# Optimization experiments

Measured on AMD Instinct MI355X. Metric: run time of the kernel, lower is better.

## Reference

```python
import jax, jax.numpy as jnp
import numpy as np

D_MODEL = 2048
RANK = 64
BATCH = 16384


def setup_inputs() -> dict:
    key = jax.random.key(0)
    ks = jax.random.split(key, 10)
    s = 1.0 / np.sqrt(D_MODEL)
    x = jax.random.normal(ks[0], (BATCH, D_MODEL), dtype=jnp.float32)
    state_re = jax.random.normal(ks[1], (BATCH, RANK), dtype=jnp.float32)
    state_im = jax.random.normal(ks[2], (BATCH, RANK), dtype=jnp.float32)
    W_dt = jax.random.uniform(ks[3], (RANK, D_MODEL), jnp.float32, -s, s)
    b_dt = jax.random.uniform(ks[4], (RANK,), jnp.float32, -s, s)
    W_ph = jax.random.uniform(ks[5], (RANK, D_MODEL), jnp.float32, -s, s)
    b_ph = jax.random.uniform(ks[6], (RANK,), jnp.float32, -s, s)
    W_B = jax.random.uniform(ks[7], (RANK, D_MODEL), jnp.float32, -s, s)
    sC = 1.0 / np.sqrt(RANK)
    W_C = jax.random.uniform(ks[8], (D_MODEL, RANK), jnp.float32, -sC, sC)
    A_real = jnp.log(jnp.arange(1, RANK + 1, dtype=jnp.float32))
    A_imag = jax.random.normal(ks[9], (RANK,), dtype=jnp.float32)
    return {"x": x, "state_re": state_re, "state_im": state_im,
            "W_dt": W_dt, "b_dt": b_dt, "W_ph": W_ph, "b_ph": b_ph,
            "W_B": W_B, "W_C": W_C, "A_real": A_real, "A_imag": A_imag}


def reference(x, state_re, state_im, W_dt, b_dt, W_ph, b_ph, W_B, W_C, A_real, A_imag):
    # four small GEMMs: [B, d_model] x [d_model, rank]
    dt = jax.nn.softplus(x @ W_dt.T + b_dt)                 # [B, rank]
    phase = jnp.tanh(x @ W_ph.T + b_ph) * jnp.pi            # [B, rank]
    decay = jnp.exp(-dt * jnp.exp(A_real))                  # [B, rank]
    angle = dt * A_imag + phase                              # [B, rank]
    B_val = x @ W_B.T                                        # [B, rank]
    cos = jnp.cos(angle)
    sin = jnp.sin(angle)
    # complex rotate-and-decay state update
    new_re = (state_re * cos - state_im * sin) * decay + B_val
    new_im = (state_re * sin + state_im * cos) * decay
    out = new_re @ W_C.T                                     # [B, d_model]
    return out, new_re, new_im
```

## Files before the change

### kernel.cpp

```cpp
#include <hip/hip_runtime.h>
#include <stdint.h>

#define D_MODEL 2048
#define RANK    64
#define BATCH   16384

#define BM      32
#define KSTEP   64
#define LDA     72

typedef unsigned short u16;
typedef __attribute__((ext_vector_type(8))) short  bf16x8;
typedef __attribute__((ext_vector_type(4))) float  f32x4;
typedef __attribute__((ext_vector_type(4))) unsigned short u16x4;
typedef __attribute__((ext_vector_type(8))) unsigned short u16x8;

#define P1_HI 0
#define P1_LO 393216
#define P2_HI 786432
#define P2_LO 917504

__device__ __forceinline__ u16 f2bf(float f) {
    uint32_t u = __float_as_uint(f);
    u += 0x7fffu + ((u >> 16) & 1u);
    return (u16)(u >> 16);
}
__device__ __forceinline__ float bf2f(u16 h) {
    return __uint_as_float(((uint32_t)h) << 16);
}

#define MFMA(a, b, c) __builtin_amdgcn_mfma_f32_16x16x32_bf16((a), (b), (c), 0, 0, 0)

__global__ __launch_bounds__(256) void prep_pack(
    const float* __restrict__ Wdt, const float* __restrict__ Wph,
    const float* __restrict__ WB,  const float* __restrict__ WC,
    u16* __restrict__ ws)
{
    const int t = blockIdx.x * 256 + threadIdx.x;
    const float* src;
    u16 *dhi, *dlo;
    if (t < 49152) {
        const int lane = t & 63;
        const int row  = (t >> 12) * 16 + (lane & 15);
        const int k0   = ((t >> 6) & 63) * 32 + (lane >> 4) * 8;
        src = (row < 64)  ? Wdt + row * 2048 + k0
            : (row < 128) ? Wph + (row - 64) * 2048 + k0
                          : WB  + (row - 128) * 2048 + k0;
        dhi = ws + P1_HI + t * 8;
        dlo = ws + P1_LO + t * 8;
    } else {
        const int t2   = t - 49152;
        const int lane = t2 & 63;
        const int row  = (t2 >> 7) * 16 + (lane & 15);
        const int k0   = ((t2 >> 6) & 1) * 32 + (lane >> 4) * 8;
        src = WC + row * 64 + k0;
        dhi = ws + P2_HI + t2 * 8;
        dlo = ws + P2_LO + t2 * 8;
    }
    const f32x4 a = *(const f32x4*)src;
    const f32x4 b = *(const f32x4*)(src + 4);
    u16x8 hi, lo;
    #pragma unroll
    for (int j = 0; j < 4; ++j) {
        hi[j]     = f2bf(a[j]);
        lo[j]     = f2bf(a[j] - bf2f(hi[j]));
        hi[4 + j] = f2bf(b[j]);
        lo[4 + j] = f2bf(b[j] - bf2f(hi[4 + j]));
    }
    *(u16x8*)dhi = hi;
    *(u16x8*)dlo = lo;
}

__global__ __launch_bounds__(256, 2) void mamba_fused(
    const float* __restrict__ x,
    const float* __restrict__ state_re, const float* __restrict__ state_im,
    const float* __restrict__ b_dt, const float* __restrict__ b_ph,
    const float* __restrict__ A_real, const float* __restrict__ A_imag,
    const u16* __restrict__ ws,
    float* __restrict__ dout)
{
    __shared__ __align__(16) u16 xa_hi[BM * LDA];
    __shared__ __align__(16) u16 xa_lo[BM * LDA];
    __shared__ __align__(16) u16 nr_hi[BM * LDA];
    __shared__ __align__(16) u16 nr_lo[BM * LDA];

    const u16* p1_hi = ws + P1_HI;
    const u16* p1_lo = ws + P1_LO;
    const u16* p2_hi = ws + P2_HI;
    const u16* p2_lo = ws + P2_LO;

    const int tid  = threadIdx.x;
    const int wg   = tid >> 6;
    const int lane = tid & 63;
    const int l15  = tid & 15;
    const int lg   = (tid & 63) >> 4;
    const int r0   = blockIdx.x * BM;

    const int srow = tid >> 3;
    const int skb  = (tid & 7) << 3;
    const float* xsrc = x + (size_t)(r0 + srow) * D_MODEL + skb;

    const int rb = wg * 16 + lg * 4;
    const int brow0 = r0 + l15;
    const int brow1 = r0 + 16 + l15;
    const f32x4 sre0 = *(const f32x4*)(state_re + (size_t)brow0 * RANK + rb);
    const f32x4 sre1 = *(const f32x4*)(state_re + (size_t)brow1 * RANK + rb);
    const f32x4 sim0 = *(const f32x4*)(state_im + (size_t)brow0 * RANK + rb);
    const f32x4 sim1 = *(const f32x4*)(state_im + (size_t)brow1 * RANK + rb);
    const f32x4 bdt4 = *(const f32x4*)(b_dt   + rb);
    const f32x4 bph4 = *(const f32x4*)(b_ph   + rb);
    const f32x4 Are4 = *(const f32x4*)(A_real + rb);
    const f32x4 Aim4 = *(const f32x4*)(A_imag + rb);

    f32x4 acc[3][2];
    #pragma unroll
    for (int g = 0; g < 3; ++g)
        #pragma unroll
        for (int m = 0; m < 2; ++m)
            acc[g][m] = (f32x4){0.f, 0.f, 0.f, 0.f};

    f32x4 va = *(const f32x4*)xsrc;
    f32x4 vb = *(const f32x4*)(xsrc + 4);

    for (int it = 0; it < D_MODEL / KSTEP; ++it) {
        f32x4 na = va, nb = vb;
        if (it < D_MODEL / KSTEP - 1) {
            na = *(const f32x4*)(xsrc + (it + 1) * KSTEP);
            nb = *(const f32x4*)(xsrc + (it + 1) * KSTEP + 4);
        }
        __syncthreads();
        {
            u16x4 h0, l0, h1, l1;
            #pragma unroll
            for (int j = 0; j < 4; ++j) {
                h0[j] = f2bf(va[j]);  l0[j] = f2bf(va[j] - bf2f(h0[j]));
                h1[j] = f2bf(vb[j]);  l1[j] = f2bf(vb[j] - bf2f(h1[j]));
            }
            *(u16x4*)(xa_hi + srow * LDA + skb)     = h0;
            *(u16x4*)(xa_hi + srow * LDA + skb + 4) = h1;
            *(u16x4*)(xa_lo + srow * LDA + skb)     = l0;
            *(u16x4*)(xa_lo + srow * LDA + skb + 4) = l1;
        }
        __syncthreads();
        #pragma unroll
        for (int kk = 0; kk < 2; ++kk) {
            const int klocal = kk * 32 + lg * 8;
            const bf16x8 xh0 = *(const bf16x8*)(xa_hi + l15 * LDA + klocal);
            const bf16x8 xl0 = *(const bf16x8*)(xa_lo + l15 * LDA + klocal);
            const bf16x8 xh1 = *(const bf16x8*)(xa_hi + (16 + l15) * LDA + klocal);
            const bf16x8 xl1 = *(const bf16x8*)(xa_lo + (16 + l15) * LDA + klocal);
            const int kwin = it * 2 + kk;
            #pragma unroll
            for (int g = 0; g < 3; ++g) {
                const int ntile = (g << 2) + wg;
                const size_t poff = (((size_t)ntile * 64 + kwin) * 64 + lane) * 8;
                const bf16x8 wh = *(const bf16x8*)(p1_hi + poff);
                const bf16x8 wl = *(const bf16x8*)(p1_lo + poff);
                acc[g][0] = MFMA(wh, xh0, acc[g][0]);
                acc[g][0] = MFMA(wl, xh0, acc[g][0]);
                acc[g][0] = MFMA(wh, xl0, acc[g][0]);
                acc[g][1] = MFMA(wh, xh1, acc[g][1]);
                acc[g][1] = MFMA(wl, xh1, acc[g][1]);
                acc[g][1] = MFMA(wh, xl1, acc[g][1]);
            }
        }
        va = na; vb = nb;
    }

    float* out_main = dout;
    float* out_nre  = dout + (size_t)BATCH * D_MODEL;
    float* out_nim  = out_nre + (size_t)BATCH * RANK;

    #pragma unroll
    for (int m = 0; m < 2; ++m) {
        const int   brow = m ? brow1 : brow0;
        const f32x4 sre4 = m ? sre1 : sre0;
        const f32x4 sim4 = m ? sim1 : sim0;
        f32x4 nre4, nim4;
        u16x4 nh4, nl4;
        #pragma unroll
        for (int j = 0; j < 4; ++j) {
            const float ydt = acc[0][m][j] + bdt4[j];
            const float dtv = fmaxf(ydt, 0.f) + log1pf(expf(-fabsf(ydt)));
            const float ph  = tanhf(acc[1][m][j] + bph4[j]) * 3.14159274101257324f;
            const float decay = expf(-dtv * expf(Are4[j]));
            const float angle = fmaf(dtv, Aim4[j], ph);
            float sn, cs;
            sincosf(angle, &sn, &cs);
            nre4[j] = (sre4[j] * cs - sim4[j] * sn) * decay + acc[2][m][j];
            nim4[j] = (sre4[j] * sn + sim4[j] * cs) * decay;
            const u16 h = f2bf(nre4[j]);
            nh4[j] = h;
            nl4[j] = f2bf(nre4[j] - bf2f(h));
        }
        *(f32x4*)(out_nre + (size_t)brow * RANK + rb) = nre4;
        *(f32x4*)(out_nim + (size_t)brow * RANK + rb) = nim4;
        *(u16x4*)(nr_hi + (m * 16 + l15) * LDA + rb) = nh4;
        *(u16x4*)(nr_lo + (m * 16 + l15) * LDA + rb) = nl4;
    }
    __syncthreads();

    bf16x8 nh[2][2], nl[2][2];
    #pragma unroll
    for (int m = 0; m < 2; ++m)
        #pragma unroll
        for (int kk = 0; kk < 2; ++kk) {
            const int off = (m * 16 + l15) * LDA + kk * 32 + lg * 8;
            nh[m][kk] = *(const bf16x8*)(nr_hi + off);
            nl[m][kk] = *(const bf16x8*)(nr_lo + off);
        }

    #pragma unroll 2
    for (int nt = 0; nt < 32; ++nt) {
        const int dtile = (wg << 5) + nt;
        bf16x8 ch[2], cl[2];
        #pragma unroll
        for (int kk = 0; kk < 2; ++kk) {
            const size_t poff = (((size_t)dtile * 2 + kk) * 64 + lane) * 8;
            ch[kk] = *(const bf16x8*)(p2_hi + poff);
            cl[kk] = *(const bf16x8*)(p2_lo + poff);
        }
        #pragma unroll
        for (int m = 0; m < 2; ++m) {
            f32x4 o = (f32x4){0.f, 0.f, 0.f, 0.f};
            #pragma unroll
            for (int kk = 0; kk < 2; ++kk) {
                o = MFMA(ch[kk], nh[m][kk], o);
                o = MFMA(cl[kk], nh[m][kk], o);
                o = MFMA(ch[kk], nl[m][kk], o);
            }
            const int brow = m ? brow1 : brow0;
            *(f32x4*)(out_main + (size_t)brow * D_MODEL + dtile * 16 + lg * 4) = o;
        }
    }
}

extern "C" void kernel_launch(void* const* d_in, const int* in_sizes, int n_in,
                              void* d_out, int out_size, void* d_ws, size_t ws_size,
                              hipStream_t stream)
{
    const float* x        = (const float*)d_in[0];
    const float* state_re = (const float*)d_in[1];
    const float* state_im = (const float*)d_in[2];
    const float* W_dt     = (const float*)d_in[3];
    const float* b_dt     = (const float*)d_in[4];
    const float* W_ph     = (const float*)d_in[5];
    const float* b_ph     = (const float*)d_in[6];
    const float* W_B      = (const float*)d_in[7];
    const float* W_C      = (const float*)d_in[8];
    const float* A_real   = (const float*)d_in[9];
    const float* A_imag   = (const float*)d_in[10];
    u16*   ws  = (u16*)d_ws;
    float* out = (float*)d_out;

    prep_pack<<<256, 256, 0, stream>>>(W_dt, W_ph, W_B, W_C, ws);
    mamba_fused<<<BATCH / BM, 256, 0, stream>>>(x, state_re, state_im, b_dt, b_ph,
                                                A_real, A_imag, ws, out);
}
```

Measured before the change: 361.5 us.

## Use 512-thread blocks with row-split warps and 256-wide K chunks

Each block now runs 8 waves: two row halves times four rank groups, so each wave owns one 16-row M tile instead of two. x is staged in 256-column chunks, which cuts the number of barrier pairs per block. The W_C fragments for the output GEMM are software-prefetched one tile ahead. The risk is that every weight fragment is now loaded by twice as many waves, doubling L2 traffic for the packed weights, and the larger LDS staging may limit occupancy.

```diff
diff --git a/kernel.cpp b/kernel.cpp
--- a/kernel.cpp
+++ b/kernel.cpp
@@ -6,8 +6,9 @@
 #define BATCH   16384
 
 #define BM      32
-#define KSTEP   64
-#define LDA     72
+#define CHUNK   256
+#define LDAC    264
+#define LDAN    72
 
 typedef unsigned short u16;
 typedef __attribute__((ext_vector_type(8))) short  bf16x8;
@@ -71,7 +72,7 @@
     *(u16x8*)dlo = lo;
 }
 
-__global__ __launch_bounds__(256, 2) void mamba_fused(
+__global__ __launch_bounds__(512, 4) void mamba_v3(
     const float* __restrict__ x,
     const float* __restrict__ state_re, const float* __restrict__ state_im,
     const float* __restrict__ b_dt, const float* __restrict__ b_ph,
@@ -79,10 +80,10 @@
     const u16* __restrict__ ws,
     float* __restrict__ dout)
 {
-    __shared__ __align__(16) u16 xa_hi[BM * LDA];
-    __shared__ __align__(16) u16 xa_lo[BM * LDA];
-    __shared__ __align__(16) u16 nr_hi[BM * LDA];
-    __shared__ __align__(16) u16 nr_lo[BM * LDA];
+    __shared__ __align__(16) u16 xa_hi[BM * LDAC];
+    __shared__ __align__(16) u16 xa_lo[BM * LDAC];
+    __shared__ __align__(16) u16 nr_hi[BM * LDAN];
+    __shared__ __align__(16) u16 nr_lo[BM * LDAN];
 
     const u16* p1_hi = ws + P1_HI;
     const u16* p1_lo = ws + P1_LO;
@@ -90,148 +91,151 @@
     const u16* p2_lo = ws + P2_LO;
 
     const int tid  = threadIdx.x;
-    const int wg   = tid >> 6;
+    const int w    = tid >> 6;
+    const int wm   = w >> 2;
+    const int wg   = w & 3;
     const int lane = tid & 63;
     const int l15  = tid & 15;
-    const int lg   = (tid & 63) >> 4;
+    const int lg   = lane >> 4;
     const int r0   = blockIdx.x * BM;
 
-    const int srow = tid >> 3;
-    const int skb  = (tid & 7) << 3;
-    const float* xsrc = x + (size_t)(r0 + srow) * D_MODEL + skb;
-
-    const int rb = wg * 16 + lg * 4;
-    const int brow0 = r0 + l15;
-    const int brow1 = r0 + 16 + l15;
-    const f32x4 sre0 = *(const f32x4*)(state_re + (size_t)brow0 * RANK + rb);
-    const f32x4 sre1 = *(const f32x4*)(state_re + (size_t)brow1 * RANK + rb);
-    const f32x4 sim0 = *(const f32x4*)(state_im + (size_t)brow0 * RANK + rb);
-    const f32x4 sim1 = *(const f32x4*)(state_im + (size_t)brow1 * RANK + rb);
+    const int srow = tid >> 4;
+    const int skc  = (tid & 15) << 4;
+    const float* xsrc = x + (size_t)(r0 + srow) * D_MODEL + skc;
+
+    const int brow_l = wm * 16 + l15;
+    const int brow   = r0 + brow_l;
+    const int rb     = wg * 16 + lg * 4;
+
+    f32x4 acc[3];
+    #pragma unroll
+    for (int g = 0; g < 3; ++g) acc[g] = (f32x4){0.f, 0.f, 0.f, 0.f};
+
+    f32x4 vx0 = *(const f32x4*)(xsrc);
+    f32x4 vx1 = *(const f32x4*)(xsrc + 4);
+    f32x4 vx2 = *(const f32x4*)(xsrc + 8);
+    f32x4 vx3 = *(const f32x4*)(xsrc + 12);
+
+    for (int c = 0; c < D_MODEL / CHUNK; ++c) {
+        __syncthreads();
+        {
+            u16x4 h, l;
+            #pragma unroll
+            for (int j = 0; j < 4; ++j) { h[j]=f2bf(vx0[j]); l[j]=f2bf(vx0[j]-bf2f(h[j])); }
+            *(u16x4*)(xa_hi + srow * LDAC + skc)      = h;
+            *(u16x4*)(xa_lo + srow * LDAC + skc)      = l;
+            #pragma unroll
+            for (int j = 0; j < 4; ++j) { h[j]=f2bf(vx1[j]); l[j]=f2bf(vx1[j]-bf2f(h[j])); }
+            *(u16x4*)(xa_hi + srow * LDAC + skc + 4)  = h;
+            *(u16x4*)(xa_lo + srow * LDAC + skc + 4)  = l;
+            #pragma unroll
+            for (int j = 0; j < 4; ++j) { h[j]=f2bf(vx2[j]); l[j]=f2bf(vx2[j]-bf2f(h[j])); }
+            *(u16x4*)(xa_hi + srow * LDAC + skc + 8)  = h;
+            *(u16x4*)(xa_lo + srow * LDAC + skc + 8)  = l;
+            #pragma unroll
+            for (int j = 0; j < 4; ++j) { h[j]=f2bf(vx3[j]); l[j]=f2bf(vx3[j]-bf2f(h[j])); }
+            *(u16x4*)(xa_hi + srow * LDAC + skc + 12) = h;
+            *(u16x4*)(xa_lo + srow * LDAC + skc + 12) = l;
+        }
+        __syncthreads();
+        if (c < D_MODEL / CHUNK - 1) {
+            const float* nsrc = xsrc + (c + 1) * CHUNK;
+            vx0 = *(const f32x4*)(nsrc);
+            vx1 = *(const f32x4*)(nsrc + 4);
+            vx2 = *(const f32x4*)(nsrc + 8);
+            vx3 = *(const f32x4*)(nsrc + 12);
+        }
+        #pragma unroll 2
+        for (int kw = 0; kw < CHUNK / 32; ++kw) {
+            const int xoff = brow_l * LDAC + kw * 32 + lg * 8;
+            const bf16x8 xh = *(const bf16x8*)(xa_hi + xoff);
+            const bf16x8 xl = *(const bf16x8*)(xa_lo + xoff);
+            const int kwin = c * (CHUNK / 32) + kw;
+            #pragma unroll
+            for (int g = 0; g < 3; ++g) {
+                const size_t poff = (((size_t)((g << 2) + wg) * 64 + kwin) * 64 + lane) * 8;
+                const bf16x8 wh = *(const bf16x8*)(p1_hi + poff);
+                const bf16x8 wl = *(const bf16x8*)(p1_lo + poff);
+                acc[g] = MFMA(wh, xh, acc[g]);
+                acc[g] = MFMA(wl, xh, acc[g]);
+                acc[g] = MFMA(wh, xl, acc[g]);
+            }
+        }
+    }
+
+    float* out_main = dout;
+    float* out_nre  = dout + (size_t)BATCH * D_MODEL;
+    float* out_nim  = out_nre + (size_t)BATCH * RANK;
+
+    const f32x4 sre4 = *(const f32x4*)(state_re + (size_t)brow * RANK + rb);
+    const f32x4 sim4 = *(const f32x4*)(state_im + (size_t)brow * RANK + rb);
     const f32x4 bdt4 = *(const f32x4*)(b_dt   + rb);
     const f32x4 bph4 = *(const f32x4*)(b_ph   + rb);
     const f32x4 Are4 = *(const f32x4*)(A_real + rb);
     const f32x4 Aim4 = *(const f32x4*)(A_imag + rb);
 
-    f32x4 acc[3][2];
-    #pragma unroll
-    for (int g = 0; g < 3; ++g)
-        #pragma unroll
-        for (int m = 0; m < 2; ++m)
-            acc[g][m] = (f32x4){0.f, 0.f, 0.f, 0.f};
-
-    f32x4 va = *(const f32x4*)xsrc;
-    f32x4 vb = *(const f32x4*)(xsrc + 4);
-
-    for (int it = 0; it < D_MODEL / KSTEP; ++it) {
-        f32x4 na = va, nb = vb;
-        if (it < D_MODEL / KSTEP - 1) {
-            na = *(const f32x4*)(xsrc + (it + 1) * KSTEP);
-            nb = *(const f32x4*)(xsrc + (it + 1) * KSTEP + 4);
-        }
-        __syncthreads();
-        {
-            u16x4 h0, l0, h1, l1;
-            #pragma unroll
-            for (int j = 0; j < 4; ++j) {
-                h0[j] = f2bf(va[j]);  l0[j] = f2bf(va[j] - bf2f(h0[j]));
-                h1[j] = f2bf(vb[j]);  l1[j] = f2bf(vb[j] - bf2f(h1[j]));
-            }
-            *(u16x4*)(xa_hi + srow * LDA + skb)     = h0;
-            *(u16x4*)(xa_hi + srow * LDA + skb + 4) = h1;
-            *(u16x4*)(xa_lo + srow * LDA + skb)     = l0;
-            *(u16x4*)(xa_lo + srow * LDA + skb + 4) = l1;
-        }
-        __syncthreads();
+    f32x4 nre4, nim4;
+    u16x4 nh4, nl4;
+    #pragma unroll
+    for (int j = 0; j < 4; ++j) {
+        const float ydt = acc[0][j] + bdt4[j];
+        const float dtv = fmaxf(ydt, 0.f) + log1pf(expf(-fabsf(ydt)));
+        const float ph  = tanhf(acc[1][j] + bph4[j]) * 3.14159274101257324f;
+        const float decay = expf(-dtv * expf(Are4[j]));
+        const float angle = fmaf(dtv, Aim4[j], ph);
+        float sn, cs;
+        sincosf(angle, &sn, &cs);
+        nre4[j] = (sre4[j] * cs - sim4[j] * sn) * decay + acc[2][j];
+        nim4[j] = (sre4[j] * sn + sim4[j] * cs) * decay;
+        const u16 h = f2bf(nre4[j]);
+        nh4[j] = h;
+        nl4[j] = f2bf(nre4[j] - bf2f(h));
+    }
+    *(f32x4*)(out_nre + (size_t)brow * RANK + rb) = nre4;
+    *(f32x4*)(out_nim + (size_t)brow * RANK + rb) = nim4;
+    *(u16x4*)(nr_hi + brow_l * LDAN + rb) = nh4;
+    *(u16x4*)(nr_lo + brow_l * LDAN + rb) = nl4;
+    __syncthreads();
+
+    bf16x8 nh[2], nl[2];
+    #pragma unroll
+    for (int kk = 0; kk < 2; ++kk) {
+        const int off = brow_l * LDAN + kk * 32 + lg * 8;
+        nh[kk] = *(const bf16x8*)(nr_hi + off);
+        nl[kk] = *(const bf16x8*)(nr_lo + off);
+    }
+
+    bf16x8 ch[2], cl[2], chn[2], cln[2];
+    {
+        const int dtile0 = wg << 5;
         #pragma unroll
         for (int kk = 0; kk < 2; ++kk) {
-            const int klocal = kk * 32 + lg * 8;
-            const bf16x8 xh0 = *(const bf16x8*)(xa_hi + l15 * LDA + klocal);
-            const bf16x8 xl0 = *(const bf16x8*)(xa_lo + l15 * LDA + klocal);
-            const bf16x8 xh1 = *(const bf16x8*)(xa_hi + (16 + l15) * LDA + klocal);
-            const bf16x8 xl1 = *(const bf16x8*)(xa_lo + (16 + l15) * LDA + klocal);
-            const int kwin = it * 2 + kk;
-            #pragma unroll
-            for (int g = 0; g < 3; ++g) {
-                const int ntile = (g << 2) + wg;
-                const size_t poff = (((size_t)ntile * 64 + kwin) * 64 + lane) * 8;
-                const bf16x8 wh = *(const bf16x8*)(p1_hi + poff);
-                const bf16x8 wl = *(const bf16x8*)(p1_lo + poff);
-                acc[g][0] = MFMA(wh, xh0, acc[g][0]);
-                acc[g][0] = MFMA(wl, xh0, acc[g][0]);
-                acc[g][0] = MFMA(wh, xl0, acc[g][0]);
-                acc[g][1] = MFMA(wh, xh1, acc[g][1]);
-                acc[g][1] = MFMA(wl, xh1, acc[g][1]);
-                acc[g][1] = MFMA(wh, xl1, acc[g][1]);
+            const size_t poff = (((size_t)dtile0 * 2 + kk) * 64 + lane) * 8;
+            ch[kk] = *(const bf16x8*)(p2_hi + poff);
+            cl[kk] = *(const bf16x8*)(p2_lo + poff);
+        }
+    }
+    for (int nt = 0; nt < 32; ++nt) {
+        if (nt < 31) {
+            const int dtn = (wg << 5) + nt + 1;
+            #pragma unroll
+            for (int kk = 0; kk < 2; ++kk) {
+                const size_t poff = (((size_t)dtn * 2 + kk) * 64 + lane) * 8;
+                chn[kk] = *(const bf16x8*)(p2_hi + poff);
+                cln[kk] = *(const bf16x8*)(p2_lo + poff);
             }
         }
-        va = na; vb = nb;
-    }
-
-    float* out_main = dout;
-    float* out_nre  = dout + (size_t)BATCH * D_MODEL;
-    float* out_nim  = out_nre + (size_t)BATCH * RANK;
-
-    #pragma unroll
-    for (int m = 0; m < 2; ++m) {
-        const int   brow = m ? brow1 : brow0;
-        const f32x4 sre4 = m ? sre1 : sre0;
-        const f32x4 sim4 = m ? sim1 : sim0;
-        f32x4 nre4, nim4;
-        u16x4 nh4, nl4;
-        #pragma unroll
-        for (int j = 0; j < 4; ++j) {
-            const float ydt = acc[0][m][j] + bdt4[j];
-            const float dtv = fmaxf(ydt, 0.f) + log1pf(expf(-fabsf(ydt)));
-            const float ph  = tanhf(acc[1][m][j] + bph4[j]) * 3.14159274101257324f;
-            const float decay = expf(-dtv * expf(Are4[j]));
-            const float angle = fmaf(dtv, Aim4[j], ph);
-            float sn, cs;
-            sincosf(angle, &sn, &cs);
-            nre4[j] = (sre4[j] * cs - sim4[j] * sn) * decay + acc[2][m][j];
-            nim4[j] = (sre4[j] * sn + sim4[j] * cs) * decay;
-            const u16 h = f2bf(nre4[j]);
-            nh4[j] = h;
-            nl4[j] = f2bf(nre4[j] - bf2f(h));
-        }
-        *(f32x4*)(out_nre + (size_t)brow * RANK + rb) = nre4;
-        *(f32x4*)(out_nim + (size_t)brow * RANK + rb) = nim4;
-        *(u16x4*)(nr_hi + (m * 16 + l15) * LDA + rb) = nh4;
-        *(u16x4*)(nr_lo + (m * 16 + l15) * LDA + rb) = nl4;
-    }
-    __syncthreads();
-
-    bf16x8 nh[2][2], nl[2][2];
-    #pragma unroll
-    for (int m = 0; m < 2; ++m)
+        f32x4 o = (f32x4){0.f, 0.f, 0.f, 0.f};
         #pragma unroll
         for (int kk = 0; kk < 2; ++kk) {
-            const int off = (m * 16 + l15) * LDA + kk * 32 + lg * 8;
-            nh[m][kk] = *(const bf16x8*)(nr_hi + off);
-            nl[m][kk] = *(const bf16x8*)(nr_lo + off);
-        }
-
-    #pragma unroll 2
-    for (int nt = 0; nt < 32; ++nt) {
+            o = MFMA(ch[kk], nh[kk], o);
+            o = MFMA(cl[kk], nh[kk], o);
+            o = MFMA(ch[kk], nl[kk], o);
+        }
         const int dtile = (wg << 5) + nt;
-        bf16x8 ch[2], cl[2];
+        *(f32x4*)(out_main + (size_t)brow * D_MODEL + dtile * 16 + lg * 4) = o;
         #pragma unroll
-        for (int kk = 0; kk < 2; ++kk) {
-            const size_t poff = (((size_t)dtile * 2 + kk) * 64 + lane) * 8;
-            ch[kk] = *(const bf16x8*)(p2_hi + poff);
-            cl[kk] = *(const bf16x8*)(p2_lo + poff);
-        }
-        #pragma unroll
-        for (int m = 0; m < 2; ++m) {
-            f32x4 o = (f32x4){0.f, 0.f, 0.f, 0.f};
-            #pragma unroll
-            for (int kk = 0; kk < 2; ++kk) {
-                o = MFMA(ch[kk], nh[m][kk], o);
-                o = MFMA(cl[kk], nh[m][kk], o);
-                o = MFMA(ch[kk], nl[m][kk], o);
-            }
-            const int brow = m ? brow1 : brow0;
-            *(f32x4*)(out_main + (size_t)brow * D_MODEL + dtile * 16 + lg * 4) = o;
-        }
+        for (int kk = 0; kk < 2; ++kk) { ch[kk] = chn[kk]; cl[kk] = cln[kk]; }
     }
 }
 
@@ -254,6 +258,6 @@
     float* out = (float*)d_out;
 
     prep_pack<<<256, 256, 0, stream>>>(W_dt, W_ph, W_B, W_C, ws);
-    mamba_fused<<<BATCH / BM, 256, 0, stream>>>(x, state_re, state_im, b_dt, b_ph,
-                                                A_real, A_imag, ws, out);
-}
+    mamba_v3<<<BATCH / BM, 512, 0, stream>>>(x, state_re, state_im, b_dt, b_ph,
+                                             A_real, A_imag, ws, out);
+}
```

Measured after the change: 329.4 us. -8.9%, faster.
